# Kernel tuning notes

Measured on AMD Instinct MI355X. Metric: run time of the kernel, lower is better.

## Reference

```python
import jax, jax.numpy as jnp
import numpy as np

NT, NTRACES, NCH = 4096, 1024, 4


def setup_inputs() -> dict:
    key = jax.random.key(0)
    k1, k2 = jax.random.split(key)
    x = jax.random.normal(k1, (NT, NTRACES, NCH), dtype=jnp.float32)
    y = jax.random.normal(k2, (NT, NTRACES, NCH), dtype=jnp.float32)
    return {"x": x, "y": y}


def _quantiles(qs, cws, values):
    # quantile function of the discrete measure (values, weights with cumsum cws)
    # evaluated at cumulative-mass levels qs (POT solver_1d convention:
    # searchsorted side='left', clipped to valid index range).
    idx = jnp.clip(jnp.searchsorted(cws, qs, side="left"), 0, values.shape[0] - 1)
    return values[idx]


def _emd2_1d(xv, yv, w):
    # 1D EMD^2 (sqeuclidean ground metric, as in ot.emd2_1d defaults) between
    # atoms at positions xv with weights w and atoms at yv with weights w.
    ix = jnp.argsort(xv)
    iy = jnp.argsort(yv)
    xs, ys = xv[ix], yv[iy]            # sorted positions
    ca = jnp.cumsum(w[ix])             # cumulative source mass
    cb = jnp.cumsum(w[iy])             # cumulative target mass (equal total)
    qs = jnp.sort(jnp.concatenate([ca, cb]))  # merged mass breakpoints, (2*nt,)
    qx = _quantiles(qs, ca, xs)
    qy = _quantiles(qs, cb, ys)
    delta = jnp.diff(qs, prepend=0.0)  # mass in each segment
    return jnp.sum(delta * (qx - qy) ** 2)


def _sinkhorn_pair(xv, yv, t):
    # faithful to Sinkhorn._sinkhorn: clamp(min=0) -> cumsum -> divide by the
    # SUM of the cumsum (note: not the last element) -> 1D EMD with positions
    # (xv, yv) and weights t = arange(nt)  [positional args of ot.emd2_1d].
    xv = jnp.cumsum(jnp.clip(xv, 0.0))
    yv = jnp.cumsum(jnp.clip(yv, 0.0))
    xv = xv / jnp.sum(xv)
    yv = yv / jnp.sum(yv)
    return _emd2_1d(xv, yv, t)


def reference(x, y):
    nt = x.shape[0]
    t = jnp.arange(nt, dtype=jnp.float32)
    xf = x.reshape(nt, -1).T  # (ntraces*nchannels, nt)
    yf = y.reshape(nt, -1).T
    losses = jax.vmap(_sinkhorn_pair, in_axes=(0, 0, None))(xf, yf, t)
    return jnp.sum(losses)
```

## Files before the change

### kernel.cpp

```cpp
#include <hip/hip_runtime.h>


#define NT   4096
#define NP   4096
#define CH   64
#define LCH  64
#define BLK  256
#define RB   32

#define PCOLS 16
#define PPAD  17

__global__ __launch_bounds__(BLK) void p1_moments(
    const float* __restrict__ x, const float* __restrict__ y,
    float* __restrict__ aX, float* __restrict__ aY,
    float* __restrict__ uL, float* __restrict__ uM,
    float* __restrict__ pL, float* __restrict__ pM,
    float* __restrict__ pLL, float* __restrict__ pMM,
    float* __restrict__ pLM,
    double* __restrict__ acc, unsigned* __restrict__ cnt)
{
  if (blockIdx.x == 0 && blockIdx.y == 0 && threadIdx.x == 0) {
    *acc = 0.0;
    *cnt = 0u;
  }

  const int pv = blockIdx.x * BLK + threadIdx.x;
  const int j  = blockIdx.y;
  const int t0 = j * LCH;
  const float2* xb = (const float2*)x + (size_t)t0 * (NP / 2) + pv;
  const float2* yb = (const float2*)y + (size_t)t0 * (NP / 2) + pv;

  float cx0 = 0.f, cx1 = 0.f, cy0 = 0.f, cy1 = 0.f;
  float uL0 = 0.f, uL1 = 0.f, uM0 = 0.f, uM1 = 0.f;
  float pL0 = 0.f, pL1 = 0.f, pM0 = 0.f, pM1 = 0.f;
  float pLL0 = 0.f, pLL1 = 0.f, pMM0 = 0.f, pMM1 = 0.f;
  float pLM0 = 0.f, pLM1 = 0.f;

  for (int ib = 0; ib < LCH; ib += RB) {
    float2 xr[RB], yr[RB];
#pragma unroll
    for (int k = 0; k < RB; ++k) {
      xr[k] = xb[(size_t)(ib + k) * (NP / 2)];
      yr[k] = yb[(size_t)(ib + k) * (NP / 2)];
    }
#pragma unroll
    for (int k = 0; k < RB; ++k) {
      const float2 xv = xr[k];
      const float2 yv = yr[k];
      const float t = (float)(t0 + ib + k);

      const float lx0 = fmaxf(xv.x, 0.f), lx1 = fmaxf(xv.y, 0.f);
      const float ly0 = fmaxf(yv.x, 0.f), ly1 = fmaxf(yv.y, 0.f);

      cx0 += lx0; cy0 += ly0;
      const float tl0 = t * cx0, tm0 = t * cy0;
      pL0  += tl0;                  pM0  += tm0;
      pLL0 = fmaf(tl0, cx0, pLL0);  pMM0 = fmaf(tm0, cy0, pMM0);
      pLM0 = fmaf(tl0, cy0, pLM0);
      uL0  += cx0;                  uM0  += cy0;

      cx1 += lx1; cy1 += ly1;
      const float tl1 = t * cx1, tm1 = t * cy1;
      pL1  += tl1;                  pM1  += tm1;
      pLL1 = fmaf(tl1, cx1, pLL1);  pMM1 = fmaf(tm1, cy1, pMM1);
      pLM1 = fmaf(tl1, cy1, pLM1);
      uL1  += cx1;                  uM1  += cy1;
    }
  }

  const size_t o2 = (size_t)j * (NP / 2) + pv;
  ((float2*)aX)[o2]  = make_float2(cx0, cx1);
  ((float2*)aY)[o2]  = make_float2(cy0, cy1);
  ((float2*)uL)[o2]  = make_float2(uL0, uL1);
  ((float2*)uM)[o2]  = make_float2(uM0, uM1);
  ((float2*)pL)[o2]  = make_float2(pL0, pL1);
  ((float2*)pM)[o2]  = make_float2(pM0, pM1);
  ((float2*)pLL)[o2] = make_float2(pLL0, pLL1);
  ((float2*)pMM)[o2] = make_float2(pMM0, pMM1);
  ((float2*)pLM)[o2] = make_float2(pLM0, pLM1);
}

__global__ __launch_bounds__(BLK) void p2_loss(
    const float* __restrict__ aX, const float* __restrict__ aY,
    const float* __restrict__ uL, const float* __restrict__ uM,
    const float* __restrict__ pL, const float* __restrict__ pM,
    const float* __restrict__ pLL, const float* __restrict__ pMM,
    const float* __restrict__ pLM,
    double* __restrict__ acc, unsigned* __restrict__ cnt,
    float* __restrict__ out)
{
  __shared__ float s[9][CH][PPAD];
  __shared__ double sred[4];
  __shared__ int lastFlag;

  const int tid = threadIdx.x;
  const int p0  = blockIdx.x * PCOLS;

  {
    const int j = tid >> 2;
    const int q = tid & 3;
    const float* __restrict__ srcs[9] = {aX, aY, uL, uM, pL, pM, pLL, pMM, pLM};
#pragma unroll
    for (int a = 0; a < 9; ++a) {
      const float4 v = *(const float4*)(srcs[a] + (size_t)j * NP + p0 + 4 * q);
      s[a][j][4 * q + 0] = v.x;
      s[a][j][4 * q + 1] = v.y;
      s[a][j][4 * q + 2] = v.z;
      s[a][j][4 * q + 3] = v.w;
    }
  }
  __syncthreads();

  const int wave = tid >> 6;
  const int lane = tid & 63;

  double wsum = 0.0;

#pragma unroll
  for (int c = 0; c < 4; ++c) {
    const int col = wave * 4 + c;

    const double a  = (double)s[0][lane][col];
    const double b  = (double)s[1][lane][col];
    const double ul = (double)s[2][lane][col];
    const double um = (double)s[3][lane][col];

    double sx = a, sy = b;
    for (int d = 1; d < 64; d <<= 1) {
      const double tx = __shfl_up(sx, d, 64);
      const double ty = __shfl_up(sy, d, 64);
      if (lane >= d) { sx += tx; sy += ty; }
    }
    const double O = sx - a;
    const double P = sy - b;

    double vx = (double)LCH * O + ul;
    double vy = (double)LCH * P + um;
    for (int m = 32; m; m >>= 1) {
      vx += __shfl_xor(vx, m, 64);
      vy += __shfl_xor(vy, m, 64);
    }
    const double isx = 1.0 / vx;
    const double isy = 1.0 / vy;

    const double g   = isx * O - isy * P;
    const double Tj  = 4096.0 * (double)lane + 2016.0;
    const double sh  = isx * (double)s[4][lane][col] - isy * (double)s[5][lane][col];
    const double shh = isx * isx * (double)s[6][lane][col]
                     - 2.0 * isx * isy * (double)s[8][lane][col]
                     + isy * isy * (double)s[7][lane][col];
    double loss = g * g * Tj + 2.0 * g * sh + shh;

    for (int m = 32; m; m >>= 1) loss += __shfl_xor(loss, m, 64);
    if (lane == 0) wsum += loss;
  }

  if (lane == 0) sred[wave] = wsum;
  __syncthreads();
  if (tid == 0) {
    const double btot = (sred[0] + sred[1]) + (sred[2] + sred[3]);
    atomicAdd(acc, btot);
    __threadfence();
    const unsigned old = atomicAdd(cnt, 1u);
    lastFlag = (old == gridDim.x - 1) ? 1 : 0;
  }
  __syncthreads();
  if (lastFlag && tid == 0) {
    const double tot = atomicAdd(acc, 0.0);
    out[0] = (float)tot;
  }
}

extern "C" void kernel_launch(void* const* d_in, const int* in_sizes, int n_in,
                              void* d_out, int out_size, void* d_ws, size_t ws_size,
                              hipStream_t stream) {
  const float* x = (const float*)d_in[0];
  const float* y = (const float*)d_in[1];
  float* out = (float*)d_out;

  const size_t CNP = (size_t)CH * NP;
  char* ws = (char*)d_ws;
  float* aX  = (float*)ws; ws += CNP * sizeof(float);
  float* aY  = (float*)ws; ws += CNP * sizeof(float);
  float* uLp = (float*)ws; ws += CNP * sizeof(float);
  float* uMp = (float*)ws; ws += CNP * sizeof(float);
  float* pLp = (float*)ws; ws += CNP * sizeof(float);
  float* pMp = (float*)ws; ws += CNP * sizeof(float);
  float* pLLp = (float*)ws; ws += CNP * sizeof(float);
  float* pMMp = (float*)ws; ws += CNP * sizeof(float);
  float* pLMp = (float*)ws; ws += CNP * sizeof(float);
  double* acc = (double*)ws; ws += 64;
  unsigned* cnt = (unsigned*)ws; ws += 64;

  dim3 g1((NP / 2) / BLK, CH);
  p1_moments<<<g1, BLK, 0, stream>>>(x, y, aX, aY, uLp, uMp, pLp, pMp,
                                     pLLp, pMMp, pLMp, acc, cnt);
  p2_loss<<<NP / PCOLS, BLK, 0, stream>>>(aX, aY, uLp, uMp, pLp, pMp,
                                          pLLp, pMMp, pLMp, acc, cnt, out);
}
```

Baseline: 157.1 us.

## Split time axis into 256 short chunks and combine sub-chunk moments in pass two

Pass one now splits the time axis into 256 chunks of 16 steps instead of 64 chunks of 64. Each 1024-thread block covers all traces with float4 loads, which gives more independent work and shorter serial dependency chains. Pass two loads the 256 chunk rows in staged pairs through shared memory. Each lane merges four sub-chunks in double precision with corrected cross terms before the wave scan and reductions. This trades four times more intermediate workspace traffic and extra pass-two arithmetic for more parallelism in pass one.

```diff
diff --git a/kernel.cpp b/kernel.cpp
--- a/kernel.cpp
+++ b/kernel.cpp
@@ -3,15 +3,15 @@
 
 #define NT   4096
 #define NP   4096
-#define CH   64
-#define LCH  64
-#define BLK  256
-#define RB   32
+#define CH   256
+#define LCH  16
+#define P1B  1024
+#define SUB  4
 
 #define PCOLS 16
 #define PPAD  17
 
-__global__ __launch_bounds__(BLK) void p1_moments(
+__global__ __launch_bounds__(P1B) void p1_moments(
     const float* __restrict__ x, const float* __restrict__ y,
     float* __restrict__ aX, float* __restrict__ aY,
     float* __restrict__ uL, float* __restrict__ uM,
@@ -20,68 +20,54 @@
     float* __restrict__ pLM,
     double* __restrict__ acc, unsigned* __restrict__ cnt)
 {
-  if (blockIdx.x == 0 && blockIdx.y == 0 && threadIdx.x == 0) {
-    *acc = 0.0;
-    *cnt = 0u;
-  }
-
-  const int pv = blockIdx.x * BLK + threadIdx.x;
-  const int j  = blockIdx.y;
-  const int t0 = j * LCH;
-  const float2* xb = (const float2*)x + (size_t)t0 * (NP / 2) + pv;
-  const float2* yb = (const float2*)y + (size_t)t0 * (NP / 2) + pv;
-
-  float cx0 = 0.f, cx1 = 0.f, cy0 = 0.f, cy1 = 0.f;
-  float uL0 = 0.f, uL1 = 0.f, uM0 = 0.f, uM1 = 0.f;
-  float pL0 = 0.f, pL1 = 0.f, pM0 = 0.f, pM1 = 0.f;
-  float pLL0 = 0.f, pLL1 = 0.f, pMM0 = 0.f, pMM1 = 0.f;
-  float pLM0 = 0.f, pLM1 = 0.f;
-
-  for (int ib = 0; ib < LCH; ib += RB) {
-    float2 xr[RB], yr[RB];
-#pragma unroll
-    for (int k = 0; k < RB; ++k) {
-      xr[k] = xb[(size_t)(ib + k) * (NP / 2)];
-      yr[k] = yb[(size_t)(ib + k) * (NP / 2)];
-    }
-#pragma unroll
-    for (int k = 0; k < RB; ++k) {
-      const float2 xv = xr[k];
-      const float2 yv = yr[k];
-      const float t = (float)(t0 + ib + k);
-
-      const float lx0 = fmaxf(xv.x, 0.f), lx1 = fmaxf(xv.y, 0.f);
-      const float ly0 = fmaxf(yv.x, 0.f), ly1 = fmaxf(yv.y, 0.f);
-
-      cx0 += lx0; cy0 += ly0;
-      const float tl0 = t * cx0, tm0 = t * cy0;
-      pL0  += tl0;                  pM0  += tm0;
-      pLL0 = fmaf(tl0, cx0, pLL0);  pMM0 = fmaf(tm0, cy0, pMM0);
-      pLM0 = fmaf(tl0, cy0, pLM0);
-      uL0  += cx0;                  uM0  += cy0;
-
-      cx1 += lx1; cy1 += ly1;
-      const float tl1 = t * cx1, tm1 = t * cy1;
-      pL1  += tl1;                  pM1  += tm1;
-      pLL1 = fmaf(tl1, cx1, pLL1);  pMM1 = fmaf(tm1, cy1, pMM1);
-      pLM1 = fmaf(tl1, cy1, pLM1);
-      uL1  += cx1;                  uM1  += cy1;
-    }
-  }
-
-  const size_t o2 = (size_t)j * (NP / 2) + pv;
-  ((float2*)aX)[o2]  = make_float2(cx0, cx1);
-  ((float2*)aY)[o2]  = make_float2(cy0, cy1);
-  ((float2*)uL)[o2]  = make_float2(uL0, uL1);
-  ((float2*)uM)[o2]  = make_float2(uM0, uM1);
-  ((float2*)pL)[o2]  = make_float2(pL0, pL1);
-  ((float2*)pM)[o2]  = make_float2(pM0, pM1);
-  ((float2*)pLL)[o2] = make_float2(pLL0, pLL1);
-  ((float2*)pMM)[o2] = make_float2(pMM0, pMM1);
-  ((float2*)pLM)[o2] = make_float2(pLM0, pLM1);
+  if (blockIdx.x == 0 && threadIdx.x == 0) { *acc = 0.0; *cnt = 0u; }
+
+  const int j   = blockIdx.x;
+  const int t0  = j * LCH;
+  const int tid = threadIdx.x;
+  const float4* xb = (const float4*)x + (size_t)t0 * (NP / 4) + tid;
+  const float4* yb = (const float4*)y + (size_t)t0 * (NP / 4) + tid;
+
+  float cx[4]  = {0.f,0.f,0.f,0.f}, cy[4]  = {0.f,0.f,0.f,0.f};
+  float uLr[4] = {0.f,0.f,0.f,0.f}, uMr[4] = {0.f,0.f,0.f,0.f};
+  float pLr[4] = {0.f,0.f,0.f,0.f}, pMr[4] = {0.f,0.f,0.f,0.f};
+  float pLLr[4]= {0.f,0.f,0.f,0.f}, pMMr[4]= {0.f,0.f,0.f,0.f};
+  float pLMr[4]= {0.f,0.f,0.f,0.f};
+
+#pragma unroll 4
+  for (int i = 0; i < LCH; ++i) {
+    const float4 xv = xb[(size_t)i * (NP / 4)];
+    const float4 yv = yb[(size_t)i * (NP / 4)];
+    const float t = (float)(t0 + i);
+#define P1STEP(e, xc, yc) { \
+      const float lx = fmaxf((xc), 0.f), ly = fmaxf((yc), 0.f); \
+      cx[e] += lx; cy[e] += ly; \
+      const float tl = t * cx[e], tm = t * cy[e]; \
+      pLr[e] += tl;                   pMr[e] += tm; \
+      pLLr[e] = fmaf(tl, cx[e], pLLr[e]); \
+      pMMr[e] = fmaf(tm, cy[e], pMMr[e]); \
+      pLMr[e] = fmaf(tl, cy[e], pLMr[e]); \
+      uLr[e] += cx[e];                uMr[e] += cy[e]; }
+    P1STEP(0, xv.x, yv.x)
+    P1STEP(1, xv.y, yv.y)
+    P1STEP(2, xv.z, yv.z)
+    P1STEP(3, xv.w, yv.w)
+#undef P1STEP
+  }
+
+  const size_t o4 = (size_t)j * (NP / 4) + tid;
+  ((float4*)aX)[o4]  = make_float4(cx[0],  cx[1],  cx[2],  cx[3]);
+  ((float4*)aY)[o4]  = make_float4(cy[0],  cy[1],  cy[2],  cy[3]);
+  ((float4*)uL)[o4]  = make_float4(uLr[0], uLr[1], uLr[2], uLr[3]);
+  ((float4*)uM)[o4]  = make_float4(uMr[0], uMr[1], uMr[2], uMr[3]);
+  ((float4*)pL)[o4]  = make_float4(pLr[0], pLr[1], pLr[2], pLr[3]);
+  ((float4*)pM)[o4]  = make_float4(pMr[0], pMr[1], pMr[2], pMr[3]);
+  ((float4*)pLL)[o4] = make_float4(pLLr[0],pLLr[1],pLLr[2],pLLr[3]);
+  ((float4*)pMM)[o4] = make_float4(pMMr[0],pMMr[1],pMMr[2],pMMr[3]);
+  ((float4*)pLM)[o4] = make_float4(pLMr[0],pLMr[1],pLMr[2],pLMr[3]);
 }
 
-__global__ __launch_bounds__(BLK) void p2_loss(
+__global__ __launch_bounds__(256) void p2_loss(
     const float* __restrict__ aX, const float* __restrict__ aY,
     const float* __restrict__ uL, const float* __restrict__ uM,
     const float* __restrict__ pL, const float* __restrict__ pM,
@@ -90,73 +76,142 @@
     double* __restrict__ acc, unsigned* __restrict__ cnt,
     float* __restrict__ out)
 {
-  __shared__ float s[9][CH][PPAD];
+  __shared__ float s0[CH][PPAD];
+  __shared__ float s1[CH][PPAD];
   __shared__ double sred[4];
   __shared__ int lastFlag;
 
-  const int tid = threadIdx.x;
-  const int p0  = blockIdx.x * PCOLS;
-
-  {
-    const int j = tid >> 2;
-    const int q = tid & 3;
-    const float* __restrict__ srcs[9] = {aX, aY, uL, uM, pL, pM, pLL, pMM, pLM};
-#pragma unroll
-    for (int a = 0; a < 9; ++a) {
-      const float4 v = *(const float4*)(srcs[a] + (size_t)j * NP + p0 + 4 * q);
-      s[a][j][4 * q + 0] = v.x;
-      s[a][j][4 * q + 1] = v.y;
-      s[a][j][4 * q + 2] = v.z;
-      s[a][j][4 * q + 3] = v.w;
-    }
-  }
-  __syncthreads();
-
+  const int tid  = threadIdx.x;
+  const int p0   = blockIdx.x * PCOLS;
   const int wave = tid >> 6;
   const int lane = tid & 63;
-
-  double wsum = 0.0;
-
-#pragma unroll
-  for (int c = 0; c < 4; ++c) {
-    const int col = wave * 4 + c;
-
-    const double a  = (double)s[0][lane][col];
-    const double b  = (double)s[1][lane][col];
-    const double ul = (double)s[2][lane][col];
-    const double um = (double)s[3][lane][col];
-
-    double sx = a, sy = b;
+  const int q    = tid & 3;
+  const int r0   = tid >> 2;
+
+#define STAGE2(A, B) { \
+    __syncthreads(); \
+    for (int rr = 0; rr < 4; ++rr) { \
+      const int r = r0 + 64 * rr; \
+      const float4 va = *(const float4*)((A) + (size_t)r * NP + p0 + 4 * q); \
+      s0[r][4*q+0] = va.x; s0[r][4*q+1] = va.y; \
+      s0[r][4*q+2] = va.z; s0[r][4*q+3] = va.w; \
+      const float4 vb = *(const float4*)((B) + (size_t)r * NP + p0 + 4 * q); \
+      s1[r][4*q+0] = vb.x; s1[r][4*q+1] = vb.y; \
+      s1[r][4*q+2] = vb.z; s1[r][4*q+3] = vb.w; \
+    } \
+    __syncthreads(); }
+
+#define STAGE1(A) { \
+    __syncthreads(); \
+    for (int rr = 0; rr < 4; ++rr) { \
+      const int r = r0 + 64 * rr; \
+      const float4 va = *(const float4*)((A) + (size_t)r * NP + p0 + 4 * q); \
+      s0[r][4*q+0] = va.x; s0[r][4*q+1] = va.y; \
+      s0[r][4*q+2] = va.z; s0[r][4*q+3] = va.w; \
+    } \
+    __syncthreads(); }
+
+  float  ax[4][SUB], ay[4][SUB];
+  float  plsub[4][SUB], pmsub[4][SUB];
+  double O[4], P[4], isx[4], isy[4], loss[4];
+
+  STAGE2(aX, aY);
+#pragma unroll
+  for (int c = 0; c < 4; ++c) {
+    const int col = wave * 4 + c;
+    double A = 0.0, B = 0.0;
+#pragma unroll
+    for (int k = 0; k < SUB; ++k) {
+      ax[c][k] = s0[SUB * lane + k][col];
+      ay[c][k] = s1[SUB * lane + k][col];
+      A += (double)ax[c][k]; B += (double)ay[c][k];
+    }
+    double sx = A, sy = B;
     for (int d = 1; d < 64; d <<= 1) {
       const double tx = __shfl_up(sx, d, 64);
       const double ty = __shfl_up(sy, d, 64);
       if (lane >= d) { sx += tx; sy += ty; }
     }
-    const double O = sx - a;
-    const double P = sy - b;
-
-    double vx = (double)LCH * O + ul;
-    double vy = (double)LCH * P + um;
+    O[c] = sx - A; P[c] = sy - B;
+  }
+
+  STAGE2(uL, uM);
+#pragma unroll
+  for (int c = 0; c < 4; ++c) {
+    const int col = wave * 4 + c;
+    double U = 0.0, V = 0.0, lx = 0.0, ly = 0.0;
+#pragma unroll
+    for (int k = 0; k < SUB; ++k) {
+      U += (double)s0[SUB * lane + k][col] + 16.0 * lx;
+      V += (double)s1[SUB * lane + k][col] + 16.0 * ly;
+      lx += (double)ax[c][k]; ly += (double)ay[c][k];
+    }
+    double vx = 64.0 * O[c] + U;
+    double vy = 64.0 * P[c] + V;
     for (int m = 32; m; m >>= 1) {
       vx += __shfl_xor(vx, m, 64);
       vy += __shfl_xor(vy, m, 64);
     }
-    const double isx = 1.0 / vx;
-    const double isy = 1.0 / vy;
-
-    const double g   = isx * O - isy * P;
-    const double Tj  = 4096.0 * (double)lane + 2016.0;
-    const double sh  = isx * (double)s[4][lane][col] - isy * (double)s[5][lane][col];
-    const double shh = isx * isx * (double)s[6][lane][col]
-                     - 2.0 * isx * isy * (double)s[8][lane][col]
-                     + isy * isy * (double)s[7][lane][col];
-    double loss = g * g * Tj + 2.0 * g * sh + shh;
-
-    for (int m = 32; m; m >>= 1) loss += __shfl_xor(loss, m, 64);
-    if (lane == 0) wsum += loss;
-  }
-
-  if (lane == 0) sred[wave] = wsum;
+    isx[c] = 1.0 / vx; isy[c] = 1.0 / vy;
+    const double g = isx[c] * O[c] - isy[c] * P[c];
+    loss[c] = g * g * (4096.0 * (double)lane + 2016.0);
+  }
+
+  STAGE2(pL, pM);
+#pragma unroll
+  for (int c = 0; c < 4; ++c) {
+    const int col = wave * 4 + c;
+    double PLv = 0.0, PMv = 0.0, lx = 0.0, ly = 0.0;
+#pragma unroll
+    for (int k = 0; k < SUB; ++k) {
+      const double Ts = 256.0 * (double)(SUB * lane + k) + 120.0;
+      const float plk = s0[SUB * lane + k][col];
+      const float pmk = s1[SUB * lane + k][col];
+      plsub[c][k] = plk; pmsub[c][k] = pmk;
+      PLv += (double)plk + lx * Ts;
+      PMv += (double)pmk + ly * Ts;
+      lx += (double)ax[c][k]; ly += (double)ay[c][k];
+    }
+    const double g = isx[c] * O[c] - isy[c] * P[c];
+    loss[c] += 2.0 * g * (isx[c] * PLv - isy[c] * PMv);
+  }
+
+  STAGE2(pLL, pMM);
+#pragma unroll
+  for (int c = 0; c < 4; ++c) {
+    const int col = wave * 4 + c;
+    double PLLv = 0.0, PMMv = 0.0, lx = 0.0, ly = 0.0;
+#pragma unroll
+    for (int k = 0; k < SUB; ++k) {
+      const double Ts = 256.0 * (double)(SUB * lane + k) + 120.0;
+      PLLv += (double)s0[SUB * lane + k][col]
+            + 2.0 * lx * (double)plsub[c][k] + lx * lx * Ts;
+      PMMv += (double)s1[SUB * lane + k][col]
+            + 2.0 * ly * (double)pmsub[c][k] + ly * ly * Ts;
+      lx += (double)ax[c][k]; ly += (double)ay[c][k];
+    }
+    loss[c] += isx[c] * isx[c] * PLLv + isy[c] * isy[c] * PMMv;
+  }
+
+  STAGE1(pLM);
+#pragma unroll
+  for (int c = 0; c < 4; ++c) {
+    const int col = wave * 4 + c;
+    double PLMv = 0.0, lx = 0.0, ly = 0.0;
+#pragma unroll
+    for (int k = 0; k < SUB; ++k) {
+      const double Ts = 256.0 * (double)(SUB * lane + k) + 120.0;
+      PLMv += (double)s0[SUB * lane + k][col]
+            + lx * (double)pmsub[c][k] + ly * (double)plsub[c][k]
+            + lx * ly * Ts;
+      lx += (double)ax[c][k]; ly += (double)ay[c][k];
+    }
+    loss[c] += -2.0 * isx[c] * isy[c] * PLMv;
+  }
+
+  double L = (loss[0] + loss[1]) + (loss[2] + loss[3]);
+  for (int m = 32; m; m >>= 1) L += __shfl_xor(L, m, 64);
+  if (lane == 0) sred[wave] = L;
   __syncthreads();
   if (tid == 0) {
     const double btot = (sred[0] + sred[1]) + (sred[2] + sred[3]);
@@ -193,9 +248,8 @@
   double* acc = (double*)ws; ws += 64;
   unsigned* cnt = (unsigned*)ws; ws += 64;
 
-  dim3 g1((NP / 2) / BLK, CH);
-  p1_moments<<<g1, BLK, 0, stream>>>(x, y, aX, aY, uLp, uMp, pLp, pMp,
+  p1_moments<<<CH, P1B, 0, stream>>>(x, y, aX, aY, uLp, uMp, pLp, pMp,
                                      pLLp, pMMp, pLMp, acc, cnt);
-  p2_loss<<<NP / PCOLS, BLK, 0, stream>>>(aX, aY, uLp, uMp, pLp, pMp,
+  p2_loss<<<NP / PCOLS, 256, 0, stream>>>(aX, aY, uLp, uMp, pLp, pMp,
                                           pLLp, pMMp, pLMp, acc, cnt, out);
 }
```

Result: slower. 171.7 us (+9.3%).

## Fuse moment and loss kernels into one, keeping per-chunk moments in LDS

Applied to the files above, without the earlier changes.

Merges the two-kernel pipeline into one. Each block computes the per-chunk cumulative moments for its 16 columns directly from the inputs, stages them in shared memory, and then runs the existing scan and loss reduction. This removes the round trip of nine 1 MB intermediate arrays through global memory and one kernel launch, at the cost of a memset launch to zero the accumulators. The grid shrinks to 256 blocks of 256 threads, each reading 16-column float4 strips with a 16 KB row stride, which may lower memory parallelism and coalescing compared with the old 2048-float-wide first kernel.

```diff
diff --git a/kernel.cpp b/kernel.cpp
--- a/kernel.cpp
+++ b/kernel.cpp
@@ -6,87 +6,11 @@
 #define CH   64
 #define LCH  64
 #define BLK  256
-#define RB   32
-
 #define PCOLS 16
 #define PPAD  17
 
-__global__ __launch_bounds__(BLK) void p1_moments(
+__global__ __launch_bounds__(BLK) void sink_fused(
     const float* __restrict__ x, const float* __restrict__ y,
-    float* __restrict__ aX, float* __restrict__ aY,
-    float* __restrict__ uL, float* __restrict__ uM,
-    float* __restrict__ pL, float* __restrict__ pM,
-    float* __restrict__ pLL, float* __restrict__ pMM,
-    float* __restrict__ pLM,
-    double* __restrict__ acc, unsigned* __restrict__ cnt)
-{
-  if (blockIdx.x == 0 && blockIdx.y == 0 && threadIdx.x == 0) {
-    *acc = 0.0;
-    *cnt = 0u;
-  }
-
-  const int pv = blockIdx.x * BLK + threadIdx.x;
-  const int j  = blockIdx.y;
-  const int t0 = j * LCH;
-  const float2* xb = (const float2*)x + (size_t)t0 * (NP / 2) + pv;
-  const float2* yb = (const float2*)y + (size_t)t0 * (NP / 2) + pv;
-
-  float cx0 = 0.f, cx1 = 0.f, cy0 = 0.f, cy1 = 0.f;
-  float uL0 = 0.f, uL1 = 0.f, uM0 = 0.f, uM1 = 0.f;
-  float pL0 = 0.f, pL1 = 0.f, pM0 = 0.f, pM1 = 0.f;
-  float pLL0 = 0.f, pLL1 = 0.f, pMM0 = 0.f, pMM1 = 0.f;
-  float pLM0 = 0.f, pLM1 = 0.f;
-
-  for (int ib = 0; ib < LCH; ib += RB) {
-    float2 xr[RB], yr[RB];
-#pragma unroll
-    for (int k = 0; k < RB; ++k) {
-      xr[k] = xb[(size_t)(ib + k) * (NP / 2)];
-      yr[k] = yb[(size_t)(ib + k) * (NP / 2)];
-    }
-#pragma unroll
-    for (int k = 0; k < RB; ++k) {
-      const float2 xv = xr[k];
-      const float2 yv = yr[k];
-      const float t = (float)(t0 + ib + k);
-
-      const float lx0 = fmaxf(xv.x, 0.f), lx1 = fmaxf(xv.y, 0.f);
-      const float ly0 = fmaxf(yv.x, 0.f), ly1 = fmaxf(yv.y, 0.f);
-
-      cx0 += lx0; cy0 += ly0;
-      const float tl0 = t * cx0, tm0 = t * cy0;
-      pL0  += tl0;                  pM0  += tm0;
-      pLL0 = fmaf(tl0, cx0, pLL0);  pMM0 = fmaf(tm0, cy0, pMM0);
-      pLM0 = fmaf(tl0, cy0, pLM0);
-      uL0  += cx0;                  uM0  += cy0;
-
-      cx1 += lx1; cy1 += ly1;
-      const float tl1 = t * cx1, tm1 = t * cy1;
-      pL1  += tl1;                  pM1  += tm1;
-      pLL1 = fmaf(tl1, cx1, pLL1);  pMM1 = fmaf(tm1, cy1, pMM1);
-      pLM1 = fmaf(tl1, cy1, pLM1);
-      uL1  += cx1;                  uM1  += cy1;
-    }
-  }
-
-  const size_t o2 = (size_t)j * (NP / 2) + pv;
-  ((float2*)aX)[o2]  = make_float2(cx0, cx1);
-  ((float2*)aY)[o2]  = make_float2(cy0, cy1);
-  ((float2*)uL)[o2]  = make_float2(uL0, uL1);
-  ((float2*)uM)[o2]  = make_float2(uM0, uM1);
-  ((float2*)pL)[o2]  = make_float2(pL0, pL1);
-  ((float2*)pM)[o2]  = make_float2(pM0, pM1);
-  ((float2*)pLL)[o2] = make_float2(pLL0, pLL1);
-  ((float2*)pMM)[o2] = make_float2(pMM0, pMM1);
-  ((float2*)pLM)[o2] = make_float2(pLM0, pLM1);
-}
-
-__global__ __launch_bounds__(BLK) void p2_loss(
-    const float* __restrict__ aX, const float* __restrict__ aY,
-    const float* __restrict__ uL, const float* __restrict__ uM,
-    const float* __restrict__ pL, const float* __restrict__ pM,
-    const float* __restrict__ pLL, const float* __restrict__ pMM,
-    const float* __restrict__ pLM,
     double* __restrict__ acc, unsigned* __restrict__ cnt,
     float* __restrict__ out)
 {
@@ -96,19 +20,51 @@
 
   const int tid = threadIdx.x;
   const int p0  = blockIdx.x * PCOLS;
+  const int j   = tid >> 2;
+  const int q   = tid & 3;
+  const int t0  = j * LCH;
 
-  {
-    const int j = tid >> 2;
-    const int q = tid & 3;
-    const float* __restrict__ srcs[9] = {aX, aY, uL, uM, pL, pM, pLL, pMM, pLM};
+  const float4* xb = (const float4*)(x + (size_t)t0 * NP + p0 + 4 * q);
+  const float4* yb = (const float4*)(y + (size_t)t0 * NP + p0 + 4 * q);
+
+  float cx[4]  = {0.f,0.f,0.f,0.f}, cy[4]  = {0.f,0.f,0.f,0.f};
+  float uLr[4] = {0.f,0.f,0.f,0.f}, uMr[4] = {0.f,0.f,0.f,0.f};
+  float pLr[4] = {0.f,0.f,0.f,0.f}, pMr[4] = {0.f,0.f,0.f,0.f};
+  float pLLr[4]= {0.f,0.f,0.f,0.f}, pMMr[4]= {0.f,0.f,0.f,0.f};
+  float pLMr[4]= {0.f,0.f,0.f,0.f};
+
+#pragma unroll 8
+  for (int i = 0; i < LCH; ++i) {
+    const float4 xv = xb[(size_t)i * (NP / 4)];
+    const float4 yv = yb[(size_t)i * (NP / 4)];
+    const float t = (float)(t0 + i);
+#define P1STEP(e, xc, yc) { \
+      const float lx = fmaxf((xc), 0.f), ly = fmaxf((yc), 0.f); \
+      cx[e] += lx; cy[e] += ly; \
+      const float tl = t * cx[e], tm = t * cy[e]; \
+      pLr[e] += tl;                   pMr[e] += tm; \
+      pLLr[e] = fmaf(tl, cx[e], pLLr[e]); \
+      pMMr[e] = fmaf(tm, cy[e], pMMr[e]); \
+      pLMr[e] = fmaf(tl, cy[e], pLMr[e]); \
+      uLr[e] += cx[e];                uMr[e] += cy[e]; }
+    P1STEP(0, xv.x, yv.x)
+    P1STEP(1, xv.y, yv.y)
+    P1STEP(2, xv.z, yv.z)
+    P1STEP(3, xv.w, yv.w)
+#undef P1STEP
+  }
+
 #pragma unroll
-    for (int a = 0; a < 9; ++a) {
-      const float4 v = *(const float4*)(srcs[a] + (size_t)j * NP + p0 + 4 * q);
-      s[a][j][4 * q + 0] = v.x;
-      s[a][j][4 * q + 1] = v.y;
-      s[a][j][4 * q + 2] = v.z;
-      s[a][j][4 * q + 3] = v.w;
-    }
+  for (int e = 0; e < 4; ++e) {
+    s[0][j][4*q+e] = cx[e];
+    s[1][j][4*q+e] = cy[e];
+    s[2][j][4*q+e] = uLr[e];
+    s[3][j][4*q+e] = uMr[e];
+    s[4][j][4*q+e] = pLr[e];
+    s[5][j][4*q+e] = pMr[e];
+    s[6][j][4*q+e] = pLLr[e];
+    s[7][j][4*q+e] = pMMr[e];
+    s[8][j][4*q+e] = pLMr[e];
   }
   __syncthreads();
 
@@ -179,23 +135,11 @@
   const float* y = (const float*)d_in[1];
   float* out = (float*)d_out;
 
-  const size_t CNP = (size_t)CH * NP;
   char* ws = (char*)d_ws;
-  float* aX  = (float*)ws; ws += CNP * sizeof(float);
-  float* aY  = (float*)ws; ws += CNP * sizeof(float);
-  float* uLp = (float*)ws; ws += CNP * sizeof(float);
-  float* uMp = (float*)ws; ws += CNP * sizeof(float);
-  float* pLp = (float*)ws; ws += CNP * sizeof(float);
-  float* pMp = (float*)ws; ws += CNP * sizeof(float);
-  float* pLLp = (float*)ws; ws += CNP * sizeof(float);
-  float* pMMp = (float*)ws; ws += CNP * sizeof(float);
-  float* pLMp = (float*)ws; ws += CNP * sizeof(float);
-  double* acc = (double*)ws; ws += 64;
-  unsigned* cnt = (unsigned*)ws; ws += 64;
+  double* acc = (double*)ws;
+  unsigned* cnt = (unsigned*)(ws + 64);
 
-  dim3 g1((NP / 2) / BLK, CH);
-  p1_moments<<<g1, BLK, 0, stream>>>(x, y, aX, aY, uLp, uMp, pLp, pMp,
-                                     pLLp, pMMp, pLMp, acc, cnt);
-  p2_loss<<<NP / PCOLS, BLK, 0, stream>>>(aX, aY, uLp, uMp, pLp, pMp,
-                                          pLLp, pMMp, pLMp, acc, cnt, out);
+  hipMemsetAsync(ws, 0, 128, stream);
+
+  sink_fused<<<NP / PCOLS, BLK, 0, stream>>>(x, y, acc, cnt, out);
 }
```

New measurement: 164.9 us. 1.05x slower.
